# Optimization experiments

Hardware: AMD Instinct MI355X
Metric: run time of the kernel (lower is better)

Reference implementation:

```python
import jax, jax.numpy as jnp
import numpy as np

N_NODES = 50000
N_EDGES = 800000
IN_DIM = 128
OUT_DIM = 64


def setup_inputs() -> dict:
    key = jax.random.key(0)
    k1, k2, k3, k4, k5 = jax.random.split(key, 5)
    h = jax.random.normal(k1, (N_NODES, IN_DIM), dtype=jnp.float32)
    # Xavier-normal-ish scale for weights
    W_w = jax.random.normal(k2, (IN_DIM, OUT_DIM), dtype=jnp.float32) * (2.0 / (IN_DIM + OUT_DIM)) ** 0.5
    W_b = jnp.zeros((OUT_DIM,), dtype=jnp.float32)
    A_w = jax.random.normal(k3, (2 * OUT_DIM, 1), dtype=jnp.float32) * (2.0 / (2 * OUT_DIM + 1)) ** 0.5
    A_b = jnp.zeros((1,), dtype=jnp.float32)
    src = jax.random.randint(k4, (N_EDGES,), 0, N_NODES, dtype=jnp.int32)
    dst = jax.random.randint(k5, (N_EDGES,), 0, N_NODES, dtype=jnp.int32)
    return {"h": h, "W_w": W_w, "W_b": W_b, "A_w": A_w, "A_b": A_b, "src": src, "dst": dst}


def reference(h, W_w, W_b, A_w, A_b, src, dst):
    n = h.shape[0]
    # Node projection: Wh = W(h)
    Wh = h @ W_w + W_b  # [N, D]
    # Attention logit e_ij = LeakyReLU(A([Wh_i; Wh_j])), computed as node-level
    # partial scores gathered per edge (same math as concat-linear, far less traffic).
    a_dst = (Wh @ A_w[:OUT_DIM, 0])  # [N] -> contribution of Wh_i (dst)
    a_src = (Wh @ A_w[OUT_DIM:, 0])  # [N] -> contribution of Wh_j (src)
    e = jax.nn.leaky_relu(a_dst[dst] + a_src[src] + A_b[0], negative_slope=0.2)  # [E]
    # Segment softmax over incoming edges of each destination node (stable).
    m = jax.ops.segment_max(e, dst, num_segments=n)  # [N], -inf for isolated nodes
    m = jnp.where(jnp.isfinite(m), m, 0.0)
    ex = jnp.exp(e - m[dst])  # [E]
    den = jax.ops.segment_sum(ex, dst, num_segments=n)  # [N]
    alpha = ex / den[dst]  # [E]
    # Weighted scatter-sum aggregate: h_i = sum_j alpha_ij * Wh_j
    out = jax.ops.segment_sum(alpha[:, None] * Wh[src], dst, num_segments=n)  # [N, D]
    # Dropout (p=0.6) is identity in eval mode; omitted for determinism.
    return out
```

## Files before the change

kernel.cpp:

```cpp
#include <hip/hip_runtime.h>
#include <hip/hip_bf16.h>
#include <hip/hip_fp16.h>

#define IN_DIM 128
#define OUT_DIM 64
#define MAXDEG 64

typedef __attribute__((ext_vector_type(8))) short short8v;
typedef __attribute__((ext_vector_type(4))) float float4v;
typedef unsigned short ushort_t;
typedef unsigned int uint_t;

__device__ inline ushort_t f_to_bf16(float f) {
    uint_t x = __float_as_uint(f);
    uint_t r = (x + 0x7fffu + ((x >> 16) & 1u)) >> 16;
    return (ushort_t)r;
}

__global__ __launch_bounds__(256) void gat_fused(
    const float* __restrict__ h, const float* __restrict__ W,
    const float* __restrict__ Wb, const float* __restrict__ Aw,
    ushort_t* __restrict__ Whb, float* __restrict__ a_dst_arr,
    float* __restrict__ a_src_arr, int N,
    const int* __restrict__ dst, int* __restrict__ cnt,
    int* __restrict__ rank, int E, int HB)
{
    __shared__ ushort_t Wl[16 * 64 * 8];

    const int t = threadIdx.x;

    if ((int)blockIdx.x < HB) {
        int base = ((int)blockIdx.x * 256 + t) * 4;
        if (base + 4 <= E) {
            int4 d4 = *(const int4*)&dst[base];
            int r0 = atomicAdd(&cnt[d4.x], 1);
            int r1 = atomicAdd(&cnt[d4.y], 1);
            int r2 = atomicAdd(&cnt[d4.z], 1);
            int r3 = atomicAdd(&cnt[d4.w], 1);
            *(int4*)&rank[base] = make_int4(r0, r1, r2, r3);
        } else {
            for (int e = base; e < E; e++) rank[e] = atomicAdd(&cnt[dst[e]], 1);
        }
        return;
    }

    const int pb = (int)blockIdx.x - HB;
    {
        int f = t * 32;
        #pragma unroll
        for (int i = 0; i < 32; i++, f++) {
            int frag = f >> 9;
            int lane = (f >> 3) & 63;
            int j    = f & 7;
            int k    = (frag >> 2) * 32 + (lane >> 4) * 8 + j;
            int d    = (frag & 3) * 16 + (lane & 15);
            Wl[f] = f_to_bf16(W[k * OUT_DIM + d]);
        }
    }
    __syncthreads();

    const int wave  = t >> 6;
    const int lane  = t & 63;
    const int node0 = (pb * 4 + wave) * 16;
    if (node0 >= N) return;
    const int quad = lane >> 4;
    const int col  = lane & 15;

    const int rowc = min(node0 + col, N - 1);
    const float* __restrict__ arow = h + (size_t)rowc * IN_DIM;

    float4v acc[4];
    #pragma unroll
    for (int db = 0; db < 4; db++) acc[db] = (float4v){0.f, 0.f, 0.f, 0.f};

    #pragma unroll
    for (int kb = 0; kb < 4; kb++) {
        const float* ap = arow + kb * 32 + quad * 8;
        float4 a0 = *(const float4*)ap;
        float4 a1 = *(const float4*)(ap + 4);
        union { short8v v; ushort_t u[8]; } af;
        af.u[0] = f_to_bf16(a0.x); af.u[1] = f_to_bf16(a0.y);
        af.u[2] = f_to_bf16(a0.z); af.u[3] = f_to_bf16(a0.w);
        af.u[4] = f_to_bf16(a1.x); af.u[5] = f_to_bf16(a1.y);
        af.u[6] = f_to_bf16(a1.z); af.u[7] = f_to_bf16(a1.w);
        #pragma unroll
        for (int db = 0; db < 4; db++) {
            short8v bf = *(const short8v*)&Wl[(((kb << 2) | db) * 64 + lane) * 8];
            acc[db] = __builtin_amdgcn_mfma_f32_16x16x32_bf16(af.v, bf, acc[db], 0, 0, 0);
        }
    }

    float wbv[4], awd[4], aws[4];
    #pragma unroll
    for (int db = 0; db < 4; db++) {
        wbv[db] = Wb[db * 16 + col];
        awd[db] = Aw[db * 16 + col];
        aws[db] = Aw[OUT_DIM + db * 16 + col];
    }

    float pd[4] = {0.f, 0.f, 0.f, 0.f};
    float ps[4] = {0.f, 0.f, 0.f, 0.f};
    #pragma unroll
    for (int db = 0; db < 4; db++) {
        #pragma unroll
        for (int r = 0; r < 4; r++) {
            float v = acc[db][r] + wbv[db];
            int node = node0 + quad * 4 + r;
            if (node < N)
                Whb[(size_t)node * OUT_DIM + db * 16 + col] = f_to_bf16(v);
            pd[r] = fmaf(v, awd[db], pd[r]);
            ps[r] = fmaf(v, aws[db], ps[r]);
        }
    }
    #pragma unroll
    for (int r = 0; r < 4; r++) {
        float d_ = pd[r], s_ = ps[r];
        #pragma unroll
        for (int off = 1; off < 16; off <<= 1) {
            d_ += __shfl_xor(d_, off);
            s_ += __shfl_xor(s_, off);
        }
        int node = node0 + quad * 4 + r;
        if (col == 0 && node < N) {
            a_dst_arr[node] = d_;
            a_src_arr[node] = s_;
        }
    }
}

__global__ __launch_bounds__(256) void gat_scatter(
    const int* __restrict__ src, const int* __restrict__ dst,
    const int* __restrict__ rank,
    const float* __restrict__ a_dst_arr, const float* __restrict__ a_src_arr,
    const float* __restrict__ Ab,
    uint_t* __restrict__ csr, int E)
{
    int base = (int)(blockIdx.x * blockDim.x + threadIdx.x) * 4;
    float ab = Ab[0];
    if (base + 4 <= E) {
        int4 s4 = *(const int4*)&src[base];
        int4 t4 = *(const int4*)&dst[base];
        int4 k4 = *(const int4*)&rank[base];
        int ss[4] = {s4.x, s4.y, s4.z, s4.w};
        int tt[4] = {t4.x, t4.y, t4.z, t4.w};
        int kk[4] = {k4.x, k4.y, k4.z, k4.w};
        #pragma unroll
        for (int i = 0; i < 4; i++) {
            float v = a_dst_arr[tt[i]] + a_src_arr[ss[i]] + ab;
            v = (v > 0.0f) ? v : 0.2f * v;
            float x = __expf(v);
            uint_t rec = (((uint_t)__half_as_ushort(__float2half(x))) << 16)
                       | (uint_t)(ss[i] & 0xffff);
            if (kk[i] < MAXDEG) csr[tt[i] * MAXDEG + kk[i]] = rec;
        }
    } else {
        for (int e = base; e < E; e++) {
            int s = src[e];
            int t = dst[e];
            float v = a_dst_arr[t] + a_src_arr[s] + ab;
            v = (v > 0.0f) ? v : 0.2f * v;
            float x = __expf(v);
            uint_t rec = (((uint_t)__half_as_ushort(__float2half(x))) << 16)
                       | (uint_t)(s & 0xffff);
            if (rank[e] < MAXDEG) csr[t * MAXDEG + rank[e]] = rec;
        }
    }
}

__global__ __launch_bounds__(256) void gat_agg(
    const int* __restrict__ cnt, const uint_t* __restrict__ csr,
    const uint_t* __restrict__ Whb2, float* __restrict__ out, int N)
{
    int node = (int)((blockIdx.x * blockDim.x + threadIdx.x) >> 6);
    int lane = threadIdx.x & 63;
    if (node >= N) return;
    int u   = __builtin_amdgcn_readfirstlane(node);
    int deg = min(cnt[u], MAXDEG);
    const uint_t* __restrict__ seg = csr + (size_t)u * MAXDEG;

    int   s_l = 0;
    float w_l = 0.f;
    if (lane < deg) {
        uint_t rec = seg[lane];
        s_l = (int)(rec & 0xffffu);
        w_l = __half2float(__ushort_as_half((ushort_t)(rec >> 16)));
    }
    float ws = w_l;
    #pragma unroll
    for (int off = 1; off < 64; off <<= 1) ws += __shfl_xor(ws, off);
    float inv  = (deg > 0) ? 1.0f / ws : 0.0f;
    float al_l = w_l * inv;

    const int el = lane >> 3;
    const int dl = lane & 7;

    float acc[8];
    #pragma unroll
    for (int i = 0; i < 8; i++) acc[i] = 0.f;

    for (int j = 0; j < deg; j += 16) {
        int   e0  = j + el;
        int   e1  = j + 8 + el;
        int   ss0 = __shfl(s_l, e0);
        float al0 = __shfl(al_l, e0);
        int   ss1 = __shfl(s_l, e1);
        float al1 = __shfl(al_l, e1);
        al0 = (e0 < deg) ? al0 : 0.0f;
        al1 = (e1 < deg) ? al1 : 0.0f;
        uint4 p0 = *(const uint4*)&Whb2[(size_t)ss0 * 32 + dl * 4];
        uint4 p1 = *(const uint4*)&Whb2[(size_t)ss1 * 32 + dl * 4];
        acc[0] = fmaf(al0, __uint_as_float(p0.x << 16),        acc[0]);
        acc[1] = fmaf(al0, __uint_as_float(p0.x & 0xffff0000u), acc[1]);
        acc[2] = fmaf(al0, __uint_as_float(p0.y << 16),        acc[2]);
        acc[3] = fmaf(al0, __uint_as_float(p0.y & 0xffff0000u), acc[3]);
        acc[4] = fmaf(al0, __uint_as_float(p0.z << 16),        acc[4]);
        acc[5] = fmaf(al0, __uint_as_float(p0.z & 0xffff0000u), acc[5]);
        acc[6] = fmaf(al0, __uint_as_float(p0.w << 16),        acc[6]);
        acc[7] = fmaf(al0, __uint_as_float(p0.w & 0xffff0000u), acc[7]);
        acc[0] = fmaf(al1, __uint_as_float(p1.x << 16),        acc[0]);
        acc[1] = fmaf(al1, __uint_as_float(p1.x & 0xffff0000u), acc[1]);
        acc[2] = fmaf(al1, __uint_as_float(p1.y << 16),        acc[2]);
        acc[3] = fmaf(al1, __uint_as_float(p1.y & 0xffff0000u), acc[3]);
        acc[4] = fmaf(al1, __uint_as_float(p1.z << 16),        acc[4]);
        acc[5] = fmaf(al1, __uint_as_float(p1.z & 0xffff0000u), acc[5]);
        acc[6] = fmaf(al1, __uint_as_float(p1.w << 16),        acc[6]);
        acc[7] = fmaf(al1, __uint_as_float(p1.w & 0xffff0000u), acc[7]);
    }

    #pragma unroll
    for (int off = 8; off < 64; off <<= 1) {
        #pragma unroll
        for (int i = 0; i < 8; i++) acc[i] += __shfl_xor(acc[i], off);
    }

    if (lane < 8) {
        float4 o0 = make_float4(acc[0], acc[1], acc[2], acc[3]);
        float4 o1 = make_float4(acc[4], acc[5], acc[6], acc[7]);
        *(float4*)&out[(size_t)u * OUT_DIM + dl * 8]     = o0;
        *(float4*)&out[(size_t)u * OUT_DIM + dl * 8 + 4] = o1;
    }
}

extern "C" void kernel_launch(void* const* d_in, const int* in_sizes, int n_in,
                              void* d_out, int out_size, void* d_ws, size_t ws_size,
                              hipStream_t stream)
{
    const float* h   = (const float*)d_in[0];
    const float* W_w = (const float*)d_in[1];
    const float* W_b = (const float*)d_in[2];
    const float* A_w = (const float*)d_in[3];
    const float* A_b = (const float*)d_in[4];
    const int*   src = (const int*)d_in[5];
    const int*   dst = (const int*)d_in[6];
    float* out = (float*)d_out;

    const int N = in_sizes[0] / IN_DIM;
    const int E = in_sizes[5];

    ushort_t* Whb   = (ushort_t*)d_ws;
    float* a_dst_a  = (float*)(Whb + (size_t)N * OUT_DIM);
    float* a_src_a  = a_dst_a + N;
    int*   cnt      = (int*)(a_src_a + N);
    int*   rank     = cnt + N;
    uint_t* csr     = (uint_t*)(rank + E);

    (void)hipMemsetAsync(cnt, 0, (size_t)N * sizeof(int), stream);

    {
        int HB = (E + 1023) / 1024;
        int waves = (N + 15) / 16;
        int PB = (waves + 3) / 4;
        gat_fused<<<HB + PB, 256, 0, stream>>>(h, W_w, W_b, A_w, Whb,
                                               a_dst_a, a_src_a, N,
                                               dst, cnt, rank, E, HB);
    }
    {
        int grid = (E / 4 + 255) / 256;
        gat_scatter<<<grid, 256, 0, stream>>>(src, dst, rank, a_dst_a, a_src_a,
                                              A_b, csr, E);
    }
    {
        int grid = (N + 3) / 4;
        gat_agg<<<grid, 256, 0, stream>>>(cnt, csr, (const uint_t*)Whb, out, N);
    }
}
```

Measured before the change: 163.5 us.

## Move degree-count atomics into scatter kernel and zero counts in projection

The separate per-edge rank pass, where dst is read and atomics are issued before the projection, is removed. The scatter kernel now takes each edge's slot with an atomicAdd on cnt directly, so the rank array is no longer written or re-read. The counts are zeroed inside the projection kernel, which replaces the hipMemsetAsync. This cuts global traffic and one memset launch, but the atomic latency now sits in the scatter kernel's critical path instead of overlapping with the projection GEMM blocks.

```diff
diff --git a/kernel.cpp b/kernel.cpp
--- a/kernel.cpp
+++ b/kernel.cpp
@@ -17,34 +17,19 @@
     return (ushort_t)r;
 }
 
-__global__ __launch_bounds__(256) void gat_fused(
+__global__ __launch_bounds__(256) void gat_proj(
     const float* __restrict__ h, const float* __restrict__ W,
     const float* __restrict__ Wb, const float* __restrict__ Aw,
     ushort_t* __restrict__ Whb, float* __restrict__ a_dst_arr,
-    float* __restrict__ a_src_arr, int N,
-    const int* __restrict__ dst, int* __restrict__ cnt,
-    int* __restrict__ rank, int E, int HB)
+    float* __restrict__ a_src_arr, int* __restrict__ cnt, int N)
 {
     __shared__ ushort_t Wl[16 * 64 * 8];
 
     const int t = threadIdx.x;
 
-    if ((int)blockIdx.x < HB) {
-        int base = ((int)blockIdx.x * 256 + t) * 4;
-        if (base + 4 <= E) {
-            int4 d4 = *(const int4*)&dst[base];
-            int r0 = atomicAdd(&cnt[d4.x], 1);
-            int r1 = atomicAdd(&cnt[d4.y], 1);
-            int r2 = atomicAdd(&cnt[d4.z], 1);
-            int r3 = atomicAdd(&cnt[d4.w], 1);
-            *(int4*)&rank[base] = make_int4(r0, r1, r2, r3);
-        } else {
-            for (int e = base; e < E; e++) rank[e] = atomicAdd(&cnt[dst[e]], 1);
-        }
-        return;
-    }
-
-    const int pb = (int)blockIdx.x - HB;
+    for (int i = (int)blockIdx.x * 256 + t; i < N; i += (int)gridDim.x * 256)
+        cnt[i] = 0;
+
     {
         int f = t * 32;
         #pragma unroll
@@ -61,7 +46,7 @@
 
     const int wave  = t >> 6;
     const int lane  = t & 63;
-    const int node0 = (pb * 4 + wave) * 16;
+    const int node0 = ((int)blockIdx.x * 4 + wave) * 16;
     if (node0 >= N) return;
     const int quad = lane >> 4;
     const int col  = lane & 15;
@@ -130,20 +115,17 @@
 
 __global__ __launch_bounds__(256) void gat_scatter(
     const int* __restrict__ src, const int* __restrict__ dst,
-    const int* __restrict__ rank,
     const float* __restrict__ a_dst_arr, const float* __restrict__ a_src_arr,
     const float* __restrict__ Ab,
-    uint_t* __restrict__ csr, int E)
+    int* __restrict__ cnt, uint_t* __restrict__ csr, int E)
 {
     int base = (int)(blockIdx.x * blockDim.x + threadIdx.x) * 4;
     float ab = Ab[0];
     if (base + 4 <= E) {
         int4 s4 = *(const int4*)&src[base];
         int4 t4 = *(const int4*)&dst[base];
-        int4 k4 = *(const int4*)&rank[base];
         int ss[4] = {s4.x, s4.y, s4.z, s4.w};
         int tt[4] = {t4.x, t4.y, t4.z, t4.w};
-        int kk[4] = {k4.x, k4.y, k4.z, k4.w};
         #pragma unroll
         for (int i = 0; i < 4; i++) {
             float v = a_dst_arr[tt[i]] + a_src_arr[ss[i]] + ab;
@@ -151,7 +133,8 @@
             float x = __expf(v);
             uint_t rec = (((uint_t)__half_as_ushort(__float2half(x))) << 16)
                        | (uint_t)(ss[i] & 0xffff);
-            if (kk[i] < MAXDEG) csr[tt[i] * MAXDEG + kk[i]] = rec;
+            int r = atomicAdd(&cnt[tt[i]], 1);
+            if (r < MAXDEG) csr[tt[i] * MAXDEG + r] = rec;
         }
     } else {
         for (int e = base; e < E; e++) {
@@ -162,7 +145,8 @@
             float x = __expf(v);
             uint_t rec = (((uint_t)__half_as_ushort(__float2half(x))) << 16)
                        | (uint_t)(s & 0xffff);
-            if (rank[e] < MAXDEG) csr[t * MAXDEG + rank[e]] = rec;
+            int r = atomicAdd(&cnt[t], 1);
+            if (r < MAXDEG) csr[t * MAXDEG + r] = rec;
         }
     }
 }
@@ -261,23 +245,18 @@
     float* a_dst_a  = (float*)(Whb + (size_t)N * OUT_DIM);
     float* a_src_a  = a_dst_a + N;
     int*   cnt      = (int*)(a_src_a + N);
-    int*   rank     = cnt + N;
-    uint_t* csr     = (uint_t*)(rank + E);
-
-    (void)hipMemsetAsync(cnt, 0, (size_t)N * sizeof(int), stream);
-
-    {
-        int HB = (E + 1023) / 1024;
+    uint_t* csr     = (uint_t*)(cnt + N);
+
+    {
         int waves = (N + 15) / 16;
         int PB = (waves + 3) / 4;
-        gat_fused<<<HB + PB, 256, 0, stream>>>(h, W_w, W_b, A_w, Whb,
-                                               a_dst_a, a_src_a, N,
-                                               dst, cnt, rank, E, HB);
+        gat_proj<<<PB, 256, 0, stream>>>(h, W_w, W_b, A_w, Whb,
+                                         a_dst_a, a_src_a, cnt, N);
     }
     {
         int grid = (E / 4 + 255) / 256;
-        gat_scatter<<<grid, 256, 0, stream>>>(src, dst, rank, a_dst_a, a_src_a,
-                                              A_b, csr, E);
+        gat_scatter<<<grid, 256, 0, stream>>>(src, dst, a_dst_a, a_src_a,
+                                              A_b, cnt, csr, E);
     }
     {
         int grid = (N + 3) / 4;
```

Result: faster. 157.4 us (-3.7%).
